# Optimization experiments

Measured on AMD Instinct MI355X. Metric: run time of the kernel, lower is better.

## Reference

```python
import jax, jax.numpy as jnp
import numpy as np

N0, N1, N2, N3 = 200000, 100000, 50000, 25000
E0, E1, E2 = 1600000, 800000, 400000
IN_DIM, HID = 16, 128


def setup_inputs() -> dict:
    key = jax.random.key(0)
    ks = jax.random.split(key, 12)
    inp = {
        "features": jax.random.normal(ks[0], (N0, IN_DIM), jnp.float32),
        "W_init": jax.random.normal(ks[1], (IN_DIM, HID), jnp.float32) / np.sqrt(IN_DIM),
        "b_init": jnp.zeros((HID,), jnp.float32),
        "W_self": jax.random.normal(ks[2], (HID, HID), jnp.float32) / np.sqrt(HID),
        "b_self": jnp.zeros((HID,), jnp.float32),
        "W_neigh": jax.random.normal(ks[3], (HID, HID), jnp.float32) / np.sqrt(HID),
        "b_neigh": jnp.zeros((HID,), jnp.float32),
        "src0": jax.random.randint(ks[4], (E0,), 0, N0, jnp.int32),
        "dst0": jax.random.randint(ks[5], (E0,), 0, N1, jnp.int32),
        "src1": jax.random.randint(ks[6], (E1,), 0, N1, jnp.int32),
        "dst1": jax.random.randint(ks[7], (E1,), 0, N2, jnp.int32),
        "src2": jax.random.randint(ks[8], (E2,), 0, N2, jnp.int32),
        "dst2": jax.random.randint(ks[9], (E2,), 0, N3, jnp.int32),
        "n1": N1, "n2": N2, "n3": N3,
    }
    return inp


def _mean_agg(h_src, src, dst, n_out):
    # gather messages along edges, segment-mean into dst nodes
    msg = h_src[src]                                             # [E, HID]
    agg = jax.ops.segment_sum(msg, dst, num_segments=n_out)      # [n_out, HID]
    cnt = jax.ops.segment_sum(jnp.ones_like(dst, jnp.float32), dst, num_segments=n_out)
    return agg / jnp.maximum(cnt, 1.0)[:, None]


def reference(features, W_init, b_init, W_self, b_self, W_neigh, b_neigh,
              src0, dst0, src1, dst1, src2, dst2, n1, n2, n3):
    # h = activation(fc_init(features))
    h = jax.nn.relu(features @ W_init + b_init)                  # [N0, HID]
    blocks = [(src0, dst0, n1), (src1, dst1, n2), (src2, dst2, n3)]
    depth = len(blocks)
    for i, (src, dst, n_out) in enumerate(blocks):
        h_neigh = _mean_agg(h, src, dst, n_out)
        # SAGEConv mean, combine_type='sum': fc_self(h_dst) + fc_neigh(mean_neigh)
        h = (h[:n_out] @ W_self + b_self) + (h_neigh @ W_neigh + b_neigh)
        if i != depth - 1:
            h = jax.nn.relu(h)
    return h                                                     # [N3, HID]
```

## Files before the change

### kernel.cpp

```cpp
#include <hip/hip_runtime.h>

#define HID 128
#define CAP 64
#define SHB 9
#define NCB0 196
#define NCB1 98
#define NCB2 49
#define SUB 8
#define CS 1280
#define TILE 2048

typedef __attribute__((ext_vector_type(2))) _Float16 h2v;
typedef __attribute__((ext_vector_type(8))) _Float16 f16x8;
typedef __attribute__((ext_vector_type(4))) float f32x4;


__device__ __forceinline__ void acc8(float* s, uint4 u) {
    union { uint4 u; h2v p[4]; } w; w.u = u;
#pragma unroll
    for (int q = 0; q < 4; q++) {
        s[2 * q]     += (float)w.p[q][0];
        s[2 * q + 1] += (float)w.p[q][1];
    }
}

__device__ __forceinline__ uint4 mean_chunk(const _Float16* __restrict__ h,
                                            const int* __restrict__ sl, int deg, int c) {
    float s[8] = {0.f, 0.f, 0.f, 0.f, 0.f, 0.f, 0.f, 0.f};
    int e = 0;
    if (deg >= 8) {
        int idx[8];
#pragma unroll
        for (int k = 0; k < 8; k++) idx[k] = sl[k];
        int nxt = 8;
        while (nxt + 8 <= deg) {
            uint4 R[8];
#pragma unroll
            for (int k = 0; k < 8; k++)
                R[k] = *(const uint4*)(h + (size_t)idx[k] * HID + c * 8);
            int nidx[8];
#pragma unroll
            for (int k = 0; k < 8; k++) nidx[k] = sl[nxt + k];
#pragma unroll
            for (int k = 0; k < 8; k++) acc8(s, R[k]);
#pragma unroll
            for (int k = 0; k < 8; k++) idx[k] = nidx[k];
            nxt += 8;
        }
        uint4 R[8];
#pragma unroll
        for (int k = 0; k < 8; k++)
            R[k] = *(const uint4*)(h + (size_t)idx[k] * HID + c * 8);
#pragma unroll
        for (int k = 0; k < 8; k++) acc8(s, R[k]);
        e = nxt;
    }
    if (e + 4 <= deg) {
        uint4 R[4];
#pragma unroll
        for (int k = 0; k < 4; k++)
            R[k] = *(const uint4*)(h + (size_t)sl[e + k] * HID + c * 8);
#pragma unroll
        for (int k = 0; k < 4; k++) acc8(s, R[k]);
        e += 4;
    }
    for (; e < deg; e++)
        acc8(s, *(const uint4*)(h + (size_t)sl[e] * HID + c * 8));
    float inv = 1.0f / (float)max(deg, 1);
    union { uint4 u; h2v p[4]; } mo;
#pragma unroll
    for (int q = 0; q < 4; q++)
        mo.p[q] = (h2v){(_Float16)(s[2 * q] * inv), (_Float16)(s[2 * q + 1] * inv)};
    return mo.u;
}

template <int T>
__device__ __forceinline__ void bin_dev(
        const int* __restrict__ src, const int* __restrict__ dst, int E,
        int lb, int nblk, int* __restrict__ buf, int* __restrict__ cur, int ncb,
        int* hist, int* gbase) {
    const int EPT = TILE / T;
    const int sub = lb & (SUB - 1);
    const int ntile = (E + TILE - 1) / TILE;
    for (int t = lb; t < ntile; t += nblk) {
        const int base = t * TILE;
        const int n = min(TILE, E - base);
        for (int i = threadIdx.x; i < ncb; i += T) hist[i] = 0;
        __syncthreads();
        int eb[TILE / T], er[TILE / T], ee[TILE / T];
#pragma unroll
        for (int k = 0; k < EPT; k++) {
            int idx = k * T + threadIdx.x;
            eb[k] = -1;
            if (idx < n) {
                int d = dst[base + idx], s = src[base + idx];
                int bb = d >> SHB;
                eb[k] = bb;
                ee[k] = ((d & 511) << 18) | s;
                er[k] = atomicAdd(&hist[bb], 1);
            }
        }
        __syncthreads();
        for (int i = threadIdx.x; i < ncb; i += T)
            gbase[i] = atomicAdd(&cur[i * SUB + sub], hist[i]);
        __syncthreads();
#pragma unroll
        for (int k = 0; k < EPT; k++) {
            if (eb[k] >= 0) {
                int pos = gbase[eb[k]] + er[k];
                if (pos < CS) buf[((size_t)eb[k] * SUB + sub) * CS + pos] = ee[k];
            }
        }
        __syncthreads();
    }
}

__device__ __forceinline__ void refine_dev(
        const int* __restrict__ buf, const int* __restrict__ cur,
        int* __restrict__ ccur, int* __restrict__ csr,
        int* __restrict__ off, int* __restrict__ cnt, int N, int bb,
        int* hist, int* loff, int* wsum, int* blkbase) {
    const int tid = threadIdx.x;
    int m[SUB];
#pragma unroll
    for (int j = 0; j < SUB; j++) m[j] = min(cur[bb * SUB + j], CS);
    hist[tid] = 0;
    __syncthreads();
#pragma unroll
    for (int j = 0; j < SUB; j++) {
        const int* __restrict__ seg = buf + ((size_t)bb * SUB + j) * CS;
        for (int i = tid; i < m[j]; i += 512)
            atomicAdd(&hist[((unsigned)seg[i]) >> 18], 1);
    }
    __syncthreads();
    int v = hist[tid];
    int lane = tid & 63;
    int incl = v;
#pragma unroll
    for (int d = 1; d < 64; d <<= 1) {
        int up = __shfl_up(incl, d, 64);
        if (lane >= d) incl += up;
    }
    if (lane == 63) wsum[tid >> 6] = incl;
    __syncthreads();
    if (tid == 0) {
        int acc = 0;
#pragma unroll
        for (int i = 0; i < 8; i++) { int w = wsum[i]; wsum[i] = acc; acc += w; }
        *blkbase = atomicAdd(ccur, acc);
    }
    __syncthreads();
    int base = *blkbase + wsum[tid >> 6] + (incl - v);
    loff[tid] = base;
    const int node = (bb << SHB) + tid;
    if (node < N) { off[node] = base; cnt[node] = v; }
    __syncthreads();
    hist[tid] = 0;
    __syncthreads();
#pragma unroll
    for (int j = 0; j < SUB; j++) {
        const int* __restrict__ seg = buf + ((size_t)bb * SUB + j) * CS;
        for (int i = tid; i < m[j]; i += 512) {
            int e = seg[i];
            int dl = ((unsigned)e) >> 18;
            int p = atomicAdd(&hist[dl], 1);
            csr[loff[dl] + p] = e & 0x3FFFF;
        }
    }
}

__global__ __launch_bounds__(256) void bin0_h0(
        const int* __restrict__ src0, const int* __restrict__ dst0, int E0,
        int* __restrict__ gcur, int* __restrict__ buf0, int nbin0,
        const float* __restrict__ feat, const float* __restrict__ W_init,
        const float* __restrict__ b_init, _Float16* __restrict__ h0, int M, int nh0) {
    __shared__ int hist[NCB0];
    __shared__ int gbase[NCB0];
    if (blockIdx.x < (unsigned)nbin0) {
        bin_dev<256>(src0, dst0, E0, blockIdx.x, nbin0, buf0, gcur, NCB0, hist, gbase);
        return;
    }
    const int hbid = blockIdx.x - nbin0;
    const int tid  = threadIdx.x;
    const int lane = tid & 63;
    const int wave = tid >> 6;
    const int ln15 = lane & 15;
    const int quad = lane >> 4;

    f16x8 Bf[2];
    float bias[2];
#pragma unroll
    for (int cc = 0; cc < 2; cc++) {
        int n = (wave * 2 + cc) * 16 + ln15;
        bias[cc] = b_init[n];
        f16x8 b;
#pragma unroll
        for (int jj = 0; jj < 8; jj++) {
            int k = quad * 8 + jj;
            b[jj] = (k < 16) ? (_Float16)W_init[k * HID + n] : (_Float16)0.f;
        }
        Bf[cc] = b;
    }

    for (int row0 = hbid * 16; row0 < M; row0 += nh0 * 16) {
        const int arow = row0 + ln15;
        f16x8 A = {0, 0, 0, 0, 0, 0, 0, 0};
        if (arow < M && quad < 2) {
            const float* p = feat + (size_t)arow * 16 + quad * 8;
            float4 v0 = *(const float4*)p;
            float4 v1 = *(const float4*)(p + 4);
            A[0] = (_Float16)v0.x; A[1] = (_Float16)v0.y;
            A[2] = (_Float16)v0.z; A[3] = (_Float16)v0.w;
            A[4] = (_Float16)v1.x; A[5] = (_Float16)v1.y;
            A[6] = (_Float16)v1.z; A[7] = (_Float16)v1.w;
        }
        f32x4 acc0 = {0.f, 0.f, 0.f, 0.f};
        f32x4 acc1 = {0.f, 0.f, 0.f, 0.f};
        acc0 = __builtin_amdgcn_mfma_f32_16x16x32_f16(A, Bf[0], acc0, 0, 0, 0);
        acc1 = __builtin_amdgcn_mfma_f32_16x16x32_f16(A, Bf[1], acc1, 0, 0, 0);
#pragma unroll
        for (int cc = 0; cc < 2; cc++) {
            int col = (wave * 2 + cc) * 16 + ln15;
            f32x4 acc = cc ? acc1 : acc0;
#pragma unroll
            for (int r = 0; r < 4; r++) {
                int row = row0 + quad * 4 + r;
                if (row < M)
                    h0[(size_t)row * HID + col] = (_Float16)fmaxf(acc[r] + bias[cc], 0.f);
            }
        }
    }
}

__global__ __launch_bounds__(512) void refine0_bin12(
        const int* __restrict__ buf0, int* __restrict__ gcur, int* __restrict__ csrcur,
        int N1v, int* __restrict__ csr0, int* __restrict__ off0, int* __restrict__ cnt0,
        const int* __restrict__ src1, const int* __restrict__ dst1, int E1,
        const int* __restrict__ src2, const int* __restrict__ dst2, int E2,
        int* __restrict__ buf1, int* __restrict__ buf2, int nb1, int nb2) {
    __shared__ int hist[512];
    __shared__ int loff[512];
    __shared__ int wsum[8];
    __shared__ int blkbase;
    const int b = blockIdx.x;
    if (b < NCB0) {
        refine_dev(buf0, gcur, csrcur, csr0, off0, cnt0, N1v, b,
                   hist, loff, wsum, &blkbase);
        return;
    }
    int lb = b - NCB0;
    if (lb < nb1)
        bin_dev<512>(src1, dst1, E1, lb, nb1, buf1, gcur + NCB0 * SUB, NCB1, hist, loff);
    else
        bin_dev<512>(src2, dst2, E2, lb - nb1, nb2, buf2, gcur + (NCB0 + NCB1) * SUB, NCB2, hist, loff);
}

__global__ __launch_bounds__(512) void gather0_refine12(
        const _Float16* __restrict__ h,
        const int* __restrict__ csr0, const int* __restrict__ off0, const int* __restrict__ cnt0,
        _Float16* __restrict__ Xm, int N1v, int nRef12,
        const int* __restrict__ buf1, const int* __restrict__ buf2,
        const int* __restrict__ gcur, int* __restrict__ csrcur,
        int N2v, int N3v,
        int* __restrict__ csr1, int* __restrict__ off1, int* __restrict__ cnt1,
        int* __restrict__ csr2, int* __restrict__ off2, int* __restrict__ cnt2) {
    __shared__ int hist[512];
    __shared__ int loff[512];
    __shared__ int wsum[8];
    __shared__ int blkbase;
    const int b = blockIdx.x;
    if (b < nRef12) {
        if (b < NCB1)
            refine_dev(buf1, gcur + NCB0 * SUB, csrcur + 1, csr1, off1, cnt1, N2v, b,
                       hist, loff, wsum, &blkbase);
        else
            refine_dev(buf2, gcur + (NCB0 + NCB1) * SUB, csrcur + 2, csr2, off2, cnt2, N3v,
                       b - NCB1, hist, loff, wsum, &blkbase);
        return;
    }
    const int tid = threadIdx.x;
    const int g = tid >> 4;
    const int c = tid & 15;
    const int node = (b - nRef12) * 32 + g;
    if (node >= N1v) return;
    int deg = min(cnt0[node], CAP);
    uint4 mo = mean_chunk(h, csr0 + off0[node], deg, c);
    *(uint4*)(Xm + (size_t)node * HID + c * 8) = mo;
}

__global__ __launch_bounds__(256) void gather_mean(
        const _Float16* __restrict__ h,
        const int* __restrict__ csr,
        const int* __restrict__ off,
        const int* __restrict__ cnt,
        _Float16* __restrict__ Xm,
        int n_out) {
    const int g = threadIdx.x >> 4;
    const int c = threadIdx.x & 15;
    const int node = blockIdx.x * 16 + g;
    if (node >= n_out) return;
    int deg = min(cnt[node], CAP);
    uint4 mo = mean_chunk(h, csr + off[node], deg, c);
    *(uint4*)(Xm + (size_t)node * HID + c * 8) = mo;
}

template <bool RELU, typename OutT>
__global__ __launch_bounds__(256) void mfma_combine2(
        const _Float16* Hself, const _Float16* __restrict__ Xm,
        const float* __restrict__ Wself, const float* __restrict__ bself,
        const float* __restrict__ Wneigh, const float* __restrict__ bneigh,
        OutT* out, int M) {
    const int tid  = threadIdx.x;
    const int lane = tid & 63;
    const int wave = tid >> 6;
    const int ln15 = lane & 15;
    const int quad = lane >> 4;

    f16x8 Bf[2][8];
    float bias[2];
#pragma unroll
    for (int cc = 0; cc < 2; cc++) {
        int n = (wave * 2 + cc) * 16 + ln15;
        bias[cc] = bself[n] + bneigh[n];
#pragma unroll
        for (int s = 0; s < 8; s++) {
            f16x8 b;
#pragma unroll
            for (int jj = 0; jj < 8; jj++) {
                int k = s * 32 + quad * 8 + jj;
                float w = (k < HID) ? Wself[k * HID + n] : Wneigh[(k - HID) * HID + n];
                b[jj] = (_Float16)w;
            }
            Bf[cc][s] = b;
        }
    }

    for (int row0 = blockIdx.x * 16; row0 < M; row0 += gridDim.x * 16) {
        const int arow = row0 + ln15;
        const bool inb = arow < M;
        const _Float16* aps = Hself + (size_t)arow * HID + quad * 8;
        const _Float16* apm = Xm    + (size_t)arow * HID + quad * 8;
        f32x4 acc0 = {0.f, 0.f, 0.f, 0.f};
        f32x4 acc1 = {0.f, 0.f, 0.f, 0.f};
#pragma unroll
        for (int s = 0; s < 8; s++) {
            f16x8 A;
            if (inb) A = (s < 4) ? *(const f16x8*)(aps + s * 32)
                                 : *(const f16x8*)(apm + (s - 4) * 32);
            else     A = (f16x8){0, 0, 0, 0, 0, 0, 0, 0};
            acc0 = __builtin_amdgcn_mfma_f32_16x16x32_f16(A, Bf[0][s], acc0, 0, 0, 0);
            acc1 = __builtin_amdgcn_mfma_f32_16x16x32_f16(A, Bf[1][s], acc1, 0, 0, 0);
        }
        __syncthreads();
#pragma unroll
        for (int cc = 0; cc < 2; cc++) {
            int col = (wave * 2 + cc) * 16 + ln15;
            f32x4 acc = cc ? acc1 : acc0;
#pragma unroll
            for (int r = 0; r < 4; r++) {
                int row = row0 + quad * 4 + r;
                if (row < M) {
                    float v = acc[r] + bias[cc];
                    if (RELU) v = fmaxf(v, 0.f);
                    out[(size_t)row * HID + col] = (OutT)v;
                }
            }
        }
    }
}

extern "C" void kernel_launch(void* const* d_in, const int* in_sizes, int n_in,
                              void* d_out, int out_size, void* d_ws, size_t ws_size,
                              hipStream_t stream) {
    const float* feat    = (const float*)d_in[0];
    const float* W_init  = (const float*)d_in[1];
    const float* b_init  = (const float*)d_in[2];
    const float* W_self  = (const float*)d_in[3];
    const float* b_self  = (const float*)d_in[4];
    const float* W_neigh = (const float*)d_in[5];
    const float* b_neigh = (const float*)d_in[6];
    const int* src0 = (const int*)d_in[7];
    const int* dst0 = (const int*)d_in[8];
    const int* src1 = (const int*)d_in[9];
    const int* dst1 = (const int*)d_in[10];
    const int* src2 = (const int*)d_in[11];
    const int* dst2 = (const int*)d_in[12];

    const int N0 = in_sizes[0] / 16;
    const int E0 = in_sizes[7];
    const int E1 = in_sizes[9];
    const int E2 = in_sizes[11];
    const int N1 = 100000, N2 = 50000, N3 = 25000;

    _Float16* h  = (_Float16*)d_ws;
    _Float16* Xm = h + (size_t)N0 * HID;
    int* csr0 = (int*)(Xm + (size_t)N1 * HID);
    int* csr1 = csr0 + E0;
    int* csr2 = csr1 + E1;
    int* off0 = csr2 + E2;
    int* off1 = off0 + N1;
    int* off2 = off1 + N2;
    int* cnt0 = off2 + N3;
    int* cnt1 = cnt0 + N1;
    int* cnt2 = cnt1 + N2;
    int* gcur = cnt2 + N3;
    int* csrcur = gcur + (NCB0 + NCB1 + NCB2) * SUB;
    int* buf0 = csrcur + 3;
    int* buf1 = buf0 + (size_t)NCB0 * SUB * CS;
    int* buf2 = buf1 + (size_t)NCB1 * SUB * CS;

    hipMemsetAsync(gcur, 0, ((NCB0 + NCB1 + NCB2) * SUB + 3) * sizeof(int), stream);

    const int nbin0 = 768, nh0 = 2304;
    bin0_h0<<<nbin0 + nh0, 256, 0, stream>>>(
        src0, dst0, E0, gcur, buf0, nbin0,
        feat, W_init, b_init, h, N0, nh0);

    const int nb1 = 256, nb2 = 128;
    refine0_bin12<<<NCB0 + nb1 + nb2, 512, 0, stream>>>(
        buf0, gcur, csrcur, N1, csr0, off0, cnt0,
        src1, dst1, E1, src2, dst2, E2, buf1, buf2, nb1, nb2);

    const int nRef12 = NCB1 + NCB2;
    gather0_refine12<<<nRef12 + (N1 + 31) / 32, 512, 0, stream>>>(
        h, csr0, off0, cnt0, Xm, N1, nRef12,
        buf1, buf2, gcur, csrcur, N2, N3,
        csr1, off1, cnt1, csr2, off2, cnt2);

    mfma_combine2<true, _Float16><<<min((N1 + 15) / 16, 1568), 256, 0, stream>>>(
        h, Xm, W_self, b_self, W_neigh, b_neigh, h, N1);
    gather_mean<<<(N2 + 15) / 16, 256, 0, stream>>>(h, csr1, off1, cnt1, Xm, N2);
    mfma_combine2<true, _Float16><<<min((N2 + 15) / 16, 1568), 256, 0, stream>>>(
        h, Xm, W_self, b_self, W_neigh, b_neigh, h, N2);
    gather_mean<<<(N3 + 15) / 16, 256, 0, stream>>>(h, csr2, off2, cnt2, Xm, N3);
    mfma_combine2<false, float><<<min((N3 + 15) / 16, 1568), 256, 0, stream>>>(
        h, Xm, W_self, b_self, W_neigh, b_neigh, (float*)d_out, N3);
}
```

Baseline: 387.0 us.

## Regroup stages: bin all layers together, overlap refine with init GEMM

Edge binning for all three layers now runs in a single first kernel. CSR refinement for all layers is then fused with the initial feature projection (h0), with each 512-thread block processing two 16-row tiles. The layer-0 gather becomes a separate grid-stride kernel and no longer shares a launch with the refine of layers 1 and 2. This changes which work overlaps inside each launch, aiming for better load balance and fewer serial dependencies, while keeping the same number of launches.

```diff
diff --git a/kernel.cpp b/kernel.cpp
--- a/kernel.cpp
+++ b/kernel.cpp
@@ -169,21 +169,56 @@
     }
 }
 
-__global__ __launch_bounds__(256) void bin0_h0(
+__global__ __launch_bounds__(256) void bin_all(
         const int* __restrict__ src0, const int* __restrict__ dst0, int E0,
-        int* __restrict__ gcur, int* __restrict__ buf0, int nbin0,
+        const int* __restrict__ src1, const int* __restrict__ dst1, int E1,
+        const int* __restrict__ src2, const int* __restrict__ dst2, int E2,
+        int* __restrict__ gcur,
+        int* __restrict__ buf0, int* __restrict__ buf1, int* __restrict__ buf2,
+        int nb0, int nb1, int nb2) {
+    __shared__ int hist[NCB0];
+    __shared__ int gbase[NCB0];
+    const int b = blockIdx.x;
+    if (b < nb0)
+        bin_dev<256>(src0, dst0, E0, b, nb0, buf0, gcur, NCB0, hist, gbase);
+    else if (b < nb0 + nb1)
+        bin_dev<256>(src1, dst1, E1, b - nb0, nb1, buf1, gcur + NCB0 * SUB, NCB1, hist, gbase);
+    else
+        bin_dev<256>(src2, dst2, E2, b - nb0 - nb1, nb2, buf2, gcur + (NCB0 + NCB1) * SUB, NCB2, hist, gbase);
+}
+
+__global__ __launch_bounds__(512) void refine_h0(
+        const int* __restrict__ buf0, const int* __restrict__ buf1, const int* __restrict__ buf2,
+        const int* __restrict__ gcur, int* __restrict__ csrcur,
+        int N1v, int N2v, int N3v, int nRef,
+        int* __restrict__ csr0, int* __restrict__ off0, int* __restrict__ cnt0,
+        int* __restrict__ csr1, int* __restrict__ off1, int* __restrict__ cnt1,
+        int* __restrict__ csr2, int* __restrict__ off2, int* __restrict__ cnt2,
         const float* __restrict__ feat, const float* __restrict__ W_init,
         const float* __restrict__ b_init, _Float16* __restrict__ h0, int M, int nh0) {
-    __shared__ int hist[NCB0];
-    __shared__ int gbase[NCB0];
-    if (blockIdx.x < (unsigned)nbin0) {
-        bin_dev<256>(src0, dst0, E0, blockIdx.x, nbin0, buf0, gcur, NCB0, hist, gbase);
+    __shared__ int hist[512];
+    __shared__ int loff[512];
+    __shared__ int wsum[8];
+    __shared__ int blkbase;
+    const int tid = threadIdx.x;
+    if (blockIdx.x < (unsigned)nRef) {
+        const int gb = blockIdx.x;
+        if (gb < NCB0)
+            refine_dev(buf0, gcur, csrcur, csr0, off0, cnt0, N1v, gb,
+                       hist, loff, wsum, &blkbase);
+        else if (gb < NCB0 + NCB1)
+            refine_dev(buf1, gcur + NCB0 * SUB, csrcur + 1, csr1, off1, cnt1, N2v, gb - NCB0,
+                       hist, loff, wsum, &blkbase);
+        else
+            refine_dev(buf2, gcur + (NCB0 + NCB1) * SUB, csrcur + 2, csr2, off2, cnt2, N3v,
+                       gb - NCB0 - NCB1, hist, loff, wsum, &blkbase);
         return;
     }
-    const int hbid = blockIdx.x - nbin0;
-    const int tid  = threadIdx.x;
-    const int lane = tid & 63;
-    const int wave = tid >> 6;
+    const int hb   = blockIdx.x - nRef;
+    const int sb   = tid >> 8;
+    const int t    = tid & 255;
+    const int lane = t & 63;
+    const int wave = t >> 6;
     const int ln15 = lane & 15;
     const int quad = lane >> 4;
 
@@ -202,7 +237,7 @@
         Bf[cc] = b;
     }
 
-    for (int row0 = hbid * 16; row0 < M; row0 += nh0 * 16) {
+    for (int row0 = (hb * 2 + sb) * 16; row0 < M; row0 += nh0 * 32) {
         const int arow = row0 + ln15;
         f16x8 A = {0, 0, 0, 0, 0, 0, 0, 0};
         if (arow < M && quad < 2) {
@@ -232,76 +267,24 @@
     }
 }
 
-__global__ __launch_bounds__(512) void refine0_bin12(
-        const int* __restrict__ buf0, int* __restrict__ gcur, int* __restrict__ csrcur,
-        int N1v, int* __restrict__ csr0, int* __restrict__ off0, int* __restrict__ cnt0,
-        const int* __restrict__ src1, const int* __restrict__ dst1, int E1,
-        const int* __restrict__ src2, const int* __restrict__ dst2, int E2,
-        int* __restrict__ buf1, int* __restrict__ buf2, int nb1, int nb2) {
-    __shared__ int hist[512];
-    __shared__ int loff[512];
-    __shared__ int wsum[8];
-    __shared__ int blkbase;
-    const int b = blockIdx.x;
-    if (b < NCB0) {
-        refine_dev(buf0, gcur, csrcur, csr0, off0, cnt0, N1v, b,
-                   hist, loff, wsum, &blkbase);
-        return;
-    }
-    int lb = b - NCB0;
-    if (lb < nb1)
-        bin_dev<512>(src1, dst1, E1, lb, nb1, buf1, gcur + NCB0 * SUB, NCB1, hist, loff);
-    else
-        bin_dev<512>(src2, dst2, E2, lb - nb1, nb2, buf2, gcur + (NCB0 + NCB1) * SUB, NCB2, hist, loff);
-}
-
-__global__ __launch_bounds__(512) void gather0_refine12(
-        const _Float16* __restrict__ h,
-        const int* __restrict__ csr0, const int* __restrict__ off0, const int* __restrict__ cnt0,
-        _Float16* __restrict__ Xm, int N1v, int nRef12,
-        const int* __restrict__ buf1, const int* __restrict__ buf2,
-        const int* __restrict__ gcur, int* __restrict__ csrcur,
-        int N2v, int N3v,
-        int* __restrict__ csr1, int* __restrict__ off1, int* __restrict__ cnt1,
-        int* __restrict__ csr2, int* __restrict__ off2, int* __restrict__ cnt2) {
-    __shared__ int hist[512];
-    __shared__ int loff[512];
-    __shared__ int wsum[8];
-    __shared__ int blkbase;
-    const int b = blockIdx.x;
-    if (b < nRef12) {
-        if (b < NCB1)
-            refine_dev(buf1, gcur + NCB0 * SUB, csrcur + 1, csr1, off1, cnt1, N2v, b,
-                       hist, loff, wsum, &blkbase);
-        else
-            refine_dev(buf2, gcur + (NCB0 + NCB1) * SUB, csrcur + 2, csr2, off2, cnt2, N3v,
-                       b - NCB1, hist, loff, wsum, &blkbase);
-        return;
-    }
-    const int tid = threadIdx.x;
-    const int g = tid >> 4;
-    const int c = tid & 15;
-    const int node = (b - nRef12) * 32 + g;
-    if (node >= N1v) return;
-    int deg = min(cnt0[node], CAP);
-    uint4 mo = mean_chunk(h, csr0 + off0[node], deg, c);
-    *(uint4*)(Xm + (size_t)node * HID + c * 8) = mo;
-}
-
-__global__ __launch_bounds__(256) void gather_mean(
+__global__ __launch_bounds__(256) void gather_mean_p(
         const _Float16* __restrict__ h,
         const int* __restrict__ csr,
         const int* __restrict__ off,
         const int* __restrict__ cnt,
         _Float16* __restrict__ Xm,
-        int n_out) {
+        int n_out, int nblk) {
     const int g = threadIdx.x >> 4;
     const int c = threadIdx.x & 15;
-    const int node = blockIdx.x * 16 + g;
-    if (node >= n_out) return;
-    int deg = min(cnt[node], CAP);
-    uint4 mo = mean_chunk(h, csr + off[node], deg, c);
-    *(uint4*)(Xm + (size_t)node * HID + c * 8) = mo;
+    const int ntile = (n_out + 15) >> 4;
+    for (int t = blockIdx.x; t < ntile; t += nblk) {
+        const int node = t * 16 + g;
+        if (node < n_out) {
+            int deg = min(cnt[node], CAP);
+            uint4 mo = mean_chunk(h, csr + off[node], deg, c);
+            *(uint4*)(Xm + (size_t)node * HID + c * 8) = mo;
+        }
+    }
 }
 
 template <bool RELU, typename OutT>
@@ -411,28 +394,27 @@
 
     hipMemsetAsync(gcur, 0, ((NCB0 + NCB1 + NCB2) * SUB + 3) * sizeof(int), stream);
 
-    const int nbin0 = 768, nh0 = 2304;
-    bin0_h0<<<nbin0 + nh0, 256, 0, stream>>>(
-        src0, dst0, E0, gcur, buf0, nbin0,
+    const int nb0 = 768, nb1 = 384, nb2 = 192;
+    bin_all<<<nb0 + nb1 + nb2, 256, 0, stream>>>(
+        src0, dst0, E0, src1, dst1, E1, src2, dst2, E2,
+        gcur, buf0, buf1, buf2, nb0, nb1, nb2);
+
+    const int nRef = NCB0 + NCB1 + NCB2, nh0 = 3072;
+    refine_h0<<<nRef + nh0, 512, 0, stream>>>(
+        buf0, buf1, buf2, gcur, csrcur, N1, N2, N3, nRef,
+        csr0, off0, cnt0, csr1, off1, cnt1, csr2, off2, cnt2,
         feat, W_init, b_init, h, N0, nh0);
 
-    const int nb1 = 256, nb2 = 128;
-    refine0_bin12<<<NCB0 + nb1 + nb2, 512, 0, stream>>>(
-        buf0, gcur, csrcur, N1, csr0, off0, cnt0,
-        src1, dst1, E1, src2, dst2, E2, buf1, buf2, nb1, nb2);
-
-    const int nRef12 = NCB1 + NCB2;
-    gather0_refine12<<<nRef12 + (N1 + 31) / 32, 512, 0, stream>>>(
-        h, csr0, off0, cnt0, Xm, N1, nRef12,
-        buf1, buf2, gcur, csrcur, N2, N3,
-        csr1, off1, cnt1, csr2, off2, cnt2);
-
+    gather_mean_p<<<2048, 256, 0, stream>>>(h, csr0, off0, cnt0, Xm, N1, 2048);
     mfma_combine2<true, _Float16><<<min((N1 + 15) / 16, 1568), 256, 0, stream>>>(
         h, Xm, W_self, b_self, W_neigh, b_neigh, h, N1);
-    gather_mean<<<(N2 + 15) / 16, 256, 0, stream>>>(h, csr1, off1, cnt1, Xm, N2);
+    gather_mean_p<<<2048, 256, 0, stream>>>(h, csr1, off1, cnt1, Xm, N2, 2048);
     mfma_combine2<true, _Float16><<<min((N2 + 15) / 16, 1568), 256, 0, stream>>>(
         h, Xm, W_self, b_self, W_neigh, b_neigh, h, N2);
-    gather_mean<<<(N3 + 15) / 16, 256, 0, stream>>>(h, csr2, off2, cnt2, Xm, N3);
+    {
+        int g = (N3 + 15) / 16;
+        gather_mean_p<<<g, 256, 0, stream>>>(h, csr2, off2, cnt2, Xm, N3, g);
+    }
     mfma_combine2<false, float><<<min((N3 + 15) / 16, 1568), 256, 0, stream>>>(
         h, Xm, W_self, b_self, W_neigh, b_neigh, (float*)d_out, N3);
 }
```

Result: no change. 383.4 us (-0.9%).
